# Kernel optimization log

Hardware: AMD Instinct MI355X
Metric: run time of the kernel (lower is better)

Reference implementation:

```python
import jax, jax.numpy as jnp
import numpy as np

E = 1024   # embd_size
H = 16     # head_count
HS = E // H
B = 8
T = 1024   # seq len == input_size
EPS = 1e-5

def _ln(x, g, b):
    m = jnp.mean(x, axis=-1, keepdims=True)
    v = jnp.mean((x - m) ** 2, axis=-1, keepdims=True)
    return (x - m) * jax.lax.rsqrt(v + EPS) * g + b

def setup_inputs() -> dict:
    key = jax.random.key(0)
    ks = jax.random.split(key, 12)
    s_attn = 1.0 / np.sqrt(E)
    s_ff1 = 1.0 / np.sqrt(E)
    s_ff2 = 1.0 / np.sqrt(4 * E)
    return {
        "x": jax.random.normal(ks[0], (B, T, E), dtype=jnp.float32),
        "wq": jax.random.normal(ks[1], (H, E, HS), dtype=jnp.float32) * s_attn,
        "wk": jax.random.normal(ks[2], (H, E, HS), dtype=jnp.float32) * s_attn,
        "wv": jax.random.normal(ks[3], (H, E, HS), dtype=jnp.float32) * s_attn,
        "w_proj": jax.random.normal(ks[4], (E, E), dtype=jnp.float32) * s_attn,
        "b_proj": jnp.zeros((E,), dtype=jnp.float32),
        "w1": jax.random.normal(ks[5], (E, 4 * E), dtype=jnp.float32) * s_ff1,
        "b1": jnp.zeros((4 * E,), dtype=jnp.float32),
        "w2": jax.random.normal(ks[6], (4 * E, E), dtype=jnp.float32) * s_ff2,
        "b2": jnp.zeros((E,), dtype=jnp.float32),
        "g1": jnp.ones((E,), dtype=jnp.float32),
        "be1": jnp.zeros((E,), dtype=jnp.float32),
        "g2": jnp.ones((E,), dtype=jnp.float32),
        "be2": jnp.zeros((E,), dtype=jnp.float32),
    }

def reference(x, wq, wk, wv, w_proj, b_proj, w1, b1, w2, b2, g1, be1, g2, be2):
    Tn = x.shape[1]
    h = _ln(x, g1, be1)
    # per-head projections, batched over heads: [B,T,E] x [H,E,S] -> [B,H,T,S]
    q = jnp.einsum('bte,hes->bhts', h, wq)
    k = jnp.einsum('bte,hes->bhts', h, wk)
    v = jnp.einsum('bte,hes->bhts', h, wv)
    scores = jnp.einsum('bhts,bhus->bhtu', q, k)
    # NOTE: source multiplies by sqrt(T) (x.shape[2] of scores), not 1/sqrt(head_size)
    scores = scores * jnp.float32(Tn) ** 0.5
    causal = jnp.tril(jnp.ones((Tn, Tn), dtype=bool))
    scores = jnp.where(causal, scores, -jnp.inf)
    attn = jax.nn.softmax(scores, axis=-1)
    out = jnp.einsum('bhtu,bhus->bhts', attn, v)           # [B,H,T,S]
    out = out.transpose(0, 2, 1, 3).reshape(x.shape[0], Tn, E)  # concat heads
    out = out @ w_proj + b_proj
    x = x + out
    f = _ln(x, g2, be2)
    f = jax.nn.relu(f @ w1 + b1) @ w2 + b2
    return x + f
```

## Files before the change

kernel.cpp:

```cpp
#include <hip/hip_runtime.h>


typedef unsigned short u16;
typedef __attribute__((ext_vector_type(8))) short  bfx8;
typedef __attribute__((ext_vector_type(4))) float  f32x4;
typedef __attribute__((ext_vector_type(4))) unsigned short u16v4;

#define MFMA16 __builtin_amdgcn_mfma_f32_16x16x32_bf16

__device__ __forceinline__ u16 f2bf(float f) {
    union { float f; unsigned u; } c; c.f = f;
    unsigned r = c.u + 0x7fffu + ((c.u >> 16) & 1u);
    return (u16)(r >> 16);
}
__device__ __forceinline__ float bf2f(u16 b) {
    union { unsigned u; float f; } c; c.u = ((unsigned)b) << 16; return c.f;
}
__device__ __forceinline__ float exp2_fast(float x) {
    float r; asm("v_exp_f32 %0, %1" : "=v"(r) : "v"(x)); return r;
}

__device__ __forceinline__ void gl_lds16(const void* g, void* l) {
    void* gg = (void*)g;
    __builtin_amdgcn_global_load_lds(
        (__attribute__((address_space(1))) void*)gg,
        (__attribute__((address_space(3))) void*)l,
        16, 0, 0);
}

__global__ __launch_bounds__(256)
void transpose_split(const float* __restrict__ src, u16* __restrict__ dhi,
                     u16* __restrict__ dlo, int C, int OS,
                     size_t inBS, size_t outBS)
{
    __shared__ float t[64][65];
    const int tid = threadIdx.x;
    const float* s = src + (size_t)blockIdx.z * inBS
                   + ((size_t)blockIdx.y * 64) * C + (size_t)blockIdx.x * 64;
    const size_t obase = (size_t)blockIdx.z * outBS
                       + ((size_t)blockIdx.x * 64) * OS + (size_t)blockIdx.y * 64;
    {
        const int r = tid >> 2, c4 = (tid & 3) * 16;
#pragma unroll
        for (int k = 0; k < 4; ++k) {
            float4 f = *(const float4*)(s + (size_t)r * C + c4 + k * 4);
            t[r][c4 + k*4 + 0] = f.x; t[r][c4 + k*4 + 1] = f.y;
            t[r][c4 + k*4 + 2] = f.z; t[r][c4 + k*4 + 3] = f.w;
        }
    }
    __syncthreads();
    {
        const int c = tid >> 2, r4 = (tid & 3) * 16;
        bfx8 h0, h1, l0, l1;
#pragma unroll
        for (int k = 0; k < 8; ++k) {
            float v0 = t[r4 + k][c];
            float v1 = t[r4 + 8 + k][c];
            u16 a = f2bf(v0), b = f2bf(v1);
            h0[k] = (short)a; h1[k] = (short)b;
            l0[k] = (short)f2bf(v0 - bf2f(a));
            l1[k] = (short)f2bf(v1 - bf2f(b));
        }
        u16* d = dhi + obase + (size_t)c * OS + r4;
        *(bfx8*)d = h0; *(bfx8*)(d + 8) = h1;
        if (dlo) {
            u16* d2 = dlo + obase + (size_t)c * OS + r4;
            *(bfx8*)d2 = l0; *(bfx8*)(d2 + 8) = l1;
        }
    }
}

__global__ __launch_bounds__(256)
void transpose_v(const u16* __restrict__ v, u16* __restrict__ vT)
{
    const int ut = blockIdx.x, h = blockIdx.y, b = blockIdx.z;
    __shared__ u16 t[64][72];
    const int tid = threadIdx.x;
    {
        const int u = tid >> 2, s4 = (tid & 3) * 16;
        const u16* src = v + ((size_t)(b * 1024 + ut * 64 + u)) * 1024 + h * 64 + s4;
        bfx8 a = *(const bfx8*)src;
        bfx8 c = *(const bfx8*)(src + 8);
#pragma unroll
        for (int k = 0; k < 8; ++k) { t[u][s4 + k] = (u16)a[k]; t[u][s4 + 8 + k] = (u16)c[k]; }
    }
    __syncthreads();
    {
        const int s = tid >> 2, u4 = (tid & 3) * 16;
        bfx8 o0, o1;
#pragma unroll
        for (int k = 0; k < 8; ++k) { o0[k] = (short)t[u4 + k][s]; o1[k] = (short)t[u4 + 8 + k][s]; }
        u16* dst = vT + ((size_t)((b * 16 + h) * 64 + s)) * 1024 + ut * 64 + u4;
        *(bfx8*)dst = o0; *(bfx8*)(dst + 8) = o1;
    }
}

__global__ __launch_bounds__(256)
void ln_split(const float* __restrict__ x, const float* __restrict__ g,
              const float* __restrict__ be, u16* __restrict__ hhi,
              u16* __restrict__ hlo)
{
    const int row = blockIdx.x;
    const int tid = threadIdx.x;
    const float4 v = ((const float4*)(x + (size_t)row * 1024))[tid];
    float s  = v.x + v.y + v.z + v.w;
    float s2 = v.x*v.x + v.y*v.y + v.z*v.z + v.w*v.w;
#pragma unroll
    for (int m = 32; m >= 1; m >>= 1) {
        s  += __shfl_xor(s,  m, 64);
        s2 += __shfl_xor(s2, m, 64);
    }
    __shared__ float rs[4], rq[4];
    if ((tid & 63) == 0) { rs[tid >> 6] = s; rq[tid >> 6] = s2; }
    __syncthreads();
    s  = rs[0] + rs[1] + rs[2] + rs[3];
    s2 = rq[0] + rq[1] + rq[2] + rq[3];
    const float mean = s * (1.0f / 1024.0f);
    const float var  = s2 * (1.0f / 1024.0f) - mean * mean;
    const float inv  = rsqrtf(var + 1e-5f);
    const int col0 = tid * 4;
    float hv[4];
    hv[0] = (v.x - mean) * inv * g[col0+0] + be[col0+0];
    hv[1] = (v.y - mean) * inv * g[col0+1] + be[col0+1];
    hv[2] = (v.z - mean) * inv * g[col0+2] + be[col0+2];
    hv[3] = (v.w - mean) * inv * g[col0+3] + be[col0+3];
    u16v4 hb, lb;
#pragma unroll
    for (int k = 0; k < 4; ++k) {
        u16 a = f2bf(hv[k]);
        hb[k] = a;
        lb[k] = f2bf(hv[k] - bf2f(a));
    }
    *(u16v4*)(hhi + (size_t)row * 1024 + col0) = hb;
    if (hlo) *(u16v4*)(hlo + (size_t)row * 1024 + col0) = lb;
}

#define BM 128
#define BN 128
#define BKT 32

template<int FLAGS>
__global__ __launch_bounds__(256, 2)
void gemm_bt(const u16* __restrict__ A, const u16* __restrict__ Bt,
             void* __restrict__ Cout, const float* __restrict__ bias,
             const float* __restrict__ res, int M, int N, int K)
{
    __shared__ u16 As[BM * BKT];
    __shared__ u16 Bs[BN * BKT];
    const int tid  = threadIdx.x;
    const int lane = tid & 63, wave = tid >> 6;
    const int wr = wave >> 1, wc = wave & 1;
    const int li = lane & 15, lg = lane >> 4;
    const size_t m0 = (size_t)blockIdx.y * BM;
    const size_t n0 = (size_t)blockIdx.x * BN;
    f32x4 acc[4][4] = {};

    const int slot0 = tid, slot1 = tid + 256;
    const int r0 = slot0 >> 2, kc0 = (slot0 & 3) * 8;
    const int r1 = slot1 >> 2, kc1 = (slot1 & 3) * 8;

    for (int kt = 0; kt < K; kt += BKT) {
        __syncthreads();
        gl_lds16(A  + (m0 + r0) * K + kt + kc0, As + slot0 * 8);
        gl_lds16(Bt + (n0 + r0) * K + kt + kc0, Bs + slot0 * 8);
        gl_lds16(A  + (m0 + r1) * K + kt + kc1, As + slot1 * 8);
        gl_lds16(Bt + (n0 + r1) * K + kt + kc1, Bs + slot1 * 8);
        __syncthreads();
        bfx8 af[4], bfr[4];
#pragma unroll
        for (int i = 0; i < 4; ++i)
            af[i] = *(const bfx8*)&As[(wr * 64 + i * 16 + li) * BKT + lg * 8];
#pragma unroll
        for (int j = 0; j < 4; ++j)
            bfr[j] = *(const bfx8*)&Bs[(wc * 64 + j * 16 + li) * BKT + lg * 8];
#pragma unroll
        for (int i = 0; i < 4; ++i)
#pragma unroll
            for (int j = 0; j < 4; ++j)
                acc[i][j] = MFMA16(af[i], bfr[j], acc[i][j], 0, 0, 0);
    }

    float* Cf = (float*)Cout;
    u16*   Cb = (u16*)Cout;
#pragma unroll
    for (int i = 0; i < 4; ++i)
#pragma unroll
        for (int j = 0; j < 4; ++j)
#pragma unroll
            for (int r = 0; r < 4; ++r) {
                const size_t row = m0 + wr * 64 + i * 16 + lg * 4 + r;
                const size_t col = n0 + wc * 64 + j * 16 + li;
                float v = acc[i][j][r];
                if (FLAGS & 1) v += bias[col];
                if (FLAGS & 2) v = fmaxf(v, 0.0f);
                if (FLAGS & 4) v += res[row * (size_t)N + col];
                if (FLAGS & 8) Cf[row * (size_t)N + col] = v;
                else           Cb[row * (size_t)N + col] = f2bf(v);
            }
}

__global__ __launch_bounds__(512, 2)
void gemm8_ffn1(const u16* __restrict__ A, const u16* __restrict__ Bt,
                u16* __restrict__ C, const float* __restrict__ bias,
                int M, int N, int K)
{
    __shared__ u16 Asl[2][2][128 * 64];
    __shared__ u16 Bsl[2][2][128 * 64];
    const int tid = threadIdx.x;
    const int lane = tid & 63, wave = tid >> 6;
    const int wr = wave >> 2, wc = wave & 3;
    const int li = lane & 15, lg = lane >> 4;

    const int bid = blockIdx.x;
    const int swz = (bid & 7) * 64 + (bid >> 3);
    const int bx = swz & 15, by = swz >> 4;
    const size_t m0 = (size_t)by * 256, n0 = (size_t)bx * 256;

    char* ldsA = (char*)&Asl[0][0][0];
    char* ldsB = (char*)&Bsl[0][0][0];

    auto stageA = [&](int j, int h) {
#pragma unroll
        for (int site = 0; site < 2; ++site) {
            const int s = tid + site * 512;
            const int r = s >> 3;
            const int cb = ((s & 7) << 4) ^ ((r & 7) << 4);
            gl_lds16((const char*)(A + (m0 + h * 128 + r) * (size_t)K + (size_t)j * 64) + cb,
                     ldsA + ((j & 1) * 2 + h) * 16384 + s * 16);
        }
    };
    auto stageB = [&](int j, int h) {
#pragma unroll
        for (int site = 0; site < 2; ++site) {
            const int s = tid + site * 512;
            const int r = s >> 3;
            const int cb = ((s & 7) << 4) ^ ((r & 7) << 4);
            gl_lds16((const char*)(Bt + (n0 + h * 128 + r) * (size_t)K + (size_t)j * 64) + cb,
                     ldsB + ((j & 1) * 2 + h) * 16384 + s * 16);
        }
    };

    const int lsw = (li & 7) << 4;
    const int aHalfBase = wr * 16384;
    const int bHalfBase = (wc >> 1) * 16384;
    const int bRow0 = (wc & 1) * 64;

    f32x4 acc[8][4] = {};
    const int NT = K >> 6;
    const int NI = NT >> 1;

    stageA(0, 0); stageA(0, 1); stageB(0, 0); stageB(0, 1);
    stageB(1, 0); stageB(1, 1);
    asm volatile("s_waitcnt vmcnt(0)" ::: "memory");
    __builtin_amdgcn_sched_barrier(0);
    __builtin_amdgcn_s_barrier();
    __builtin_amdgcn_sched_barrier(0);

    for (int t = 0; t < NI; ++t) {
        const bool more = (t + 1 < NI);
#pragma unroll
        for (int half = 0; half < 2; ++half) {
            const int buf = half;
            const int abase = buf * 32768 + aHalfBase;
            const int bbase = buf * 32768 + bHalfBase;
            bfx8 bfr[4][2];
#pragma unroll
            for (int q = 0; q < 4; ++q) {
                if (q == 0) {
#pragma unroll
                    for (int nf = 0; nf < 4; ++nf)
#pragma unroll
                        for (int ks = 0; ks < 2; ++ks)
                            bfr[nf][ks] = *(const bfx8*)(ldsB + bbase
                                + (bRow0 + nf * 16 + li) * 128
                                + ((ks * 64 + lg * 16) ^ lsw));
                }
                bfx8 afr[2][2];
#pragma unroll
                for (int m = 0; m < 2; ++m)
#pragma unroll
                    for (int ks = 0; ks < 2; ++ks)
                        afr[m][ks] = *(const bfx8*)(ldsA + abase
                            + ((2 * q + m) * 16 + li) * 128
                            + ((ks * 64 + lg * 16) ^ lsw));

                if (half == 0) {
                    if (q == 0) stageA(2 * t + 1, 0);
                    else if (q == 1) stageA(2 * t + 1, 1);
                    else if (q == 2) { if (more) stageB(2 * t + 2, 0); }
                    else             { if (more) stageB(2 * t + 2, 1); }
                } else {
                    if (q == 0)      { if (more) stageA(2 * t + 2, 0); }
                    else if (q == 1) { if (more) stageA(2 * t + 2, 1); }
                    else if (q == 2) { if (more) stageB(2 * t + 3, 0); }
                    else             { if (more) stageB(2 * t + 3, 1); }
                }

                __builtin_amdgcn_sched_barrier(0);
                __builtin_amdgcn_s_barrier();
                asm volatile("s_waitcnt lgkmcnt(0)" ::: "memory");
                __builtin_amdgcn_sched_barrier(0);
                __builtin_amdgcn_s_setprio(1);
#pragma unroll
                for (int ks = 0; ks < 2; ++ks)
#pragma unroll
                    for (int m = 0; m < 2; ++m)
#pragma unroll
                        for (int nf = 0; nf < 4; ++nf)
                            acc[2 * q + m][nf] = MFMA16(afr[m][ks], bfr[nf][ks],
                                                        acc[2 * q + m][nf], 0, 0, 0);
                __builtin_amdgcn_s_setprio(0);
                __builtin_amdgcn_sched_barrier(0);
                if (q == 3) {
                    if (half == 0) {
                        if (more) { asm volatile("s_waitcnt vmcnt(4)" ::: "memory"); }
                        else      { asm volatile("s_waitcnt vmcnt(0)" ::: "memory"); }
                    } else if (more) {
                        asm volatile("s_waitcnt vmcnt(4)" ::: "memory");
                    }
                    __builtin_amdgcn_sched_barrier(0);
                }
                __builtin_amdgcn_s_barrier();
                __builtin_amdgcn_sched_barrier(0);
            }
        }
    }

#pragma unroll
    for (int i = 0; i < 8; ++i)
#pragma unroll
        for (int nf = 0; nf < 4; ++nf)
#pragma unroll
            for (int r = 0; r < 4; ++r) {
                const size_t row = m0 + wr * 128 + i * 16 + lg * 4 + r;
                const size_t col = n0 + wc * 64 + nf * 16 + li;
                float v = acc[i][nf][r] + bias[col];
                v = fmaxf(v, 0.0f);
                C[row * (size_t)N + col] = f2bf(v);
            }
}

__global__ __launch_bounds__(256, 2)
void gemm_qk(const u16* __restrict__ Ah, const u16* __restrict__ Al,
             const u16* __restrict__ Bh, const u16* __restrict__ Bl,
             u16* __restrict__ Ohi, u16* __restrict__ Olo,
             int M, int N, int K)
{
    __shared__ u16 Ahs[BM * BKT], Als[BM * BKT], Bhs[BN * BKT], Bls[BN * BKT];
    const int tid  = threadIdx.x;
    const int lane = tid & 63, wave = tid >> 6;
    const int wr = wave >> 1, wc = wave & 1;
    const int li = lane & 15, lg = lane >> 4;
    const size_t m0 = (size_t)blockIdx.y * BM;
    const size_t n0 = (size_t)blockIdx.x * BN;
    f32x4 acc[4][4] = {};

    const int slot0 = tid, slot1 = tid + 256;
    const int r0 = slot0 >> 2, kc0 = (slot0 & 3) * 8;
    const int r1 = slot1 >> 2, kc1 = (slot1 & 3) * 8;

    for (int kt = 0; kt < K; kt += BKT) {
        __syncthreads();
        gl_lds16(Ah + (m0 + r0) * K + kt + kc0, Ahs + slot0 * 8);
        gl_lds16(Al + (m0 + r0) * K + kt + kc0, Als + slot0 * 8);
        gl_lds16(Bh + (n0 + r0) * K + kt + kc0, Bhs + slot0 * 8);
        gl_lds16(Bl + (n0 + r0) * K + kt + kc0, Bls + slot0 * 8);
        gl_lds16(Ah + (m0 + r1) * K + kt + kc1, Ahs + slot1 * 8);
        gl_lds16(Al + (m0 + r1) * K + kt + kc1, Als + slot1 * 8);
        gl_lds16(Bh + (n0 + r1) * K + kt + kc1, Bhs + slot1 * 8);
        gl_lds16(Bl + (n0 + r1) * K + kt + kc1, Bls + slot1 * 8);
        __syncthreads();
        bfx8 ah[4], al4[4], bh[4], bl4[4];
#pragma unroll
        for (int i = 0; i < 4; ++i) {
            ah[i]  = *(const bfx8*)&Ahs[(wr * 64 + i * 16 + li) * BKT + lg * 8];
            al4[i] = *(const bfx8*)&Als[(wr * 64 + i * 16 + li) * BKT + lg * 8];
        }
#pragma unroll
        for (int j = 0; j < 4; ++j) {
            bh[j]  = *(const bfx8*)&Bhs[(wc * 64 + j * 16 + li) * BKT + lg * 8];
            bl4[j] = *(const bfx8*)&Bls[(wc * 64 + j * 16 + li) * BKT + lg * 8];
        }
#pragma unroll
        for (int i = 0; i < 4; ++i)
#pragma unroll
            for (int j = 0; j < 4; ++j) {
                acc[i][j] = MFMA16(ah[i],  bh[j],  acc[i][j], 0, 0, 0);
                acc[i][j] = MFMA16(ah[i],  bl4[j], acc[i][j], 0, 0, 0);
                acc[i][j] = MFMA16(al4[i], bh[j],  acc[i][j], 0, 0, 0);
            }
    }
#pragma unroll
    for (int i = 0; i < 4; ++i)
#pragma unroll
        for (int j = 0; j < 4; ++j)
#pragma unroll
            for (int r = 0; r < 4; ++r) {
                const size_t row = m0 + wr * 64 + i * 16 + lg * 4 + r;
                const size_t col = n0 + wc * 64 + j * 16 + li;
                const float v = acc[i][j][r];
                const u16 hi = f2bf(v);
                Ohi[row * (size_t)N + col] = hi;
                Olo[row * (size_t)N + col] = f2bf(v - bf2f(hi));
            }
}

#define QKS 2048

__global__ __launch_bounds__(256, 3)
void attn(const u16* __restrict__ qkhi, const u16* __restrict__ qklo,
          const u16* __restrict__ vt, u16* __restrict__ ao)
{
    const int id  = blockIdx.x;
    const int swz = (id & 7) * 256 + (id >> 3);
    const int qt  = 15 - (swz & 15);
    const int h   = (swz >> 4) & 15;
    const int b   = swz >> 8;

    const int tid = threadIdx.x;
    const int wave = tid >> 6, lane = tid & 63;
    const int li = lane & 15, lg = lane >> 4;

    __shared__ u16 KsHi[2][4096];
    __shared__ u16 KsLo[2][4096];
    __shared__ u16 Pl[64 * 64];

    const size_t qrow = (size_t)b * 1024 + qt * 64 + wave * 16 + li;
    const size_t qoff = qrow * QKS + h * 64 + lg * 8;
    const bfx8 qh0 = *(const bfx8*)(qkhi + qoff);
    const bfx8 qh1 = *(const bfx8*)(qkhi + qoff + 32);
    const bfx8 ql0 = *(const bfx8*)(qklo + qoff);
    const bfx8 ql1 = *(const bfx8*)(qklo + qoff + 32);

    bfx8 onesf;
#pragma unroll
    for (int k = 0; k < 8; ++k) onesf[k] = (short)0x3F80;

    f32x4 O[4] = {};
    f32x4 O5 = {0.f, 0.f, 0.f, 0.f};
    float mrow[4] = {-3e38f, -3e38f, -3e38f, -3e38f};

    const u16* kh_base = qkhi + ((size_t)b * 1024) * QKS + 1024 + h * 64;
    const u16* kl_base = qklo + ((size_t)b * 1024) * QKS + 1024 + h * 64;
    const u16* v_base  = vt + ((size_t)(b * 16 + h) * 64) * 1024;

    auto stageK = [&](int kt, int bufIdx) {
#pragma unroll
        for (int site = 0; site < 2; ++site) {
            const int s = tid + site * 256;
            const int r = s >> 3;
            const int cb = (((s & 7) << 4) ^ ((r & 7) << 4));
            const size_t go = ((size_t)(kt * 64 + r)) * QKS;
            gl_lds16((const char*)(kh_base + go) + cb, (char*)&KsHi[bufIdx][0] + s * 16);
            gl_lds16((const char*)(kl_base + go) + cb, (char*)&KsLo[bufIdx][0] + s * 16);
        }
    };

    const int rswz = (li & 7) << 4;
    char* pband = (char*)&Pl[0] + wave * 2048;

    stageK(0, 0);

    for (int kt = 0; kt <= qt; ++kt) {
        const int cur = kt & 1;

        bfx8 vld[2][4];
#pragma unroll
        for (int nf = 0; nf < 4; ++nf) {
            const u16* vr = v_base + ((size_t)(nf * 16 + li)) * 1024 + kt * 64 + lg * 8;
            vld[0][nf] = *(const bfx8*)vr;
            vld[1][nf] = *(const bfx8*)(vr + 32);
        }

        if (kt < qt) {
            stageK(kt + 1, cur ^ 1);
            asm volatile("s_waitcnt vmcnt(12)" ::: "memory");
        } else {
            asm volatile("s_waitcnt vmcnt(8)" ::: "memory");
        }
        __builtin_amdgcn_sched_barrier(0);
        __builtin_amdgcn_s_barrier();
        __builtin_amdgcn_sched_barrier(0);

        float sv[4][4];
        const char* khc = (const char*)&KsHi[cur][0];
        const char* klc = (const char*)&KsLo[cur][0];
#pragma unroll
        for (int nf = 0; nf < 4; ++nf) {
            const int rb = (nf * 16 + li) * 128;
            bfx8 kh0v = *(const bfx8*)(khc + rb + (((lg * 16) + 0 ) ^ rswz));
            bfx8 kh1v = *(const bfx8*)(khc + rb + (((lg * 16) + 64) ^ rswz));
            bfx8 kl0v = *(const bfx8*)(klc + rb + (((lg * 16) + 0 ) ^ rswz));
            bfx8 kl1v = *(const bfx8*)(klc + rb + (((lg * 16) + 64) ^ rswz));
            f32x4 a = {0.f, 0.f, 0.f, 0.f};
            a = MFMA16(qh0, kh0v, a, 0, 0, 0);
            a = MFMA16(qh1, kh1v, a, 0, 0, 0);
            a = MFMA16(qh0, kl0v, a, 0, 0, 0);
            a = MFMA16(qh1, kl1v, a, 0, 0, 0);
            a = MFMA16(ql0, kh0v, a, 0, 0, 0);
            a = MFMA16(ql1, kh1v, a, 0, 0, 0);
#pragma unroll
            for (int r = 0; r < 4; ++r) sv[nf][r] = a[r];
        }

        asm volatile("s_waitcnt lgkmcnt(0)" ::: "memory");
        __builtin_amdgcn_sched_barrier(0);
        __builtin_amdgcn_s_barrier();
        __builtin_amdgcn_sched_barrier(0);

        const float SC = 46.16624130844683f;
        float pmax[4] = {-3e38f, -3e38f, -3e38f, -3e38f};
        if (kt == qt) {
            const int rowg = qt * 64 + wave * 16 + lg * 4;
            const int colg = kt * 64 + li;
#pragma unroll
            for (int nf = 0; nf < 4; ++nf)
#pragma unroll
                for (int r = 0; r < 4; ++r) {
                    float x2 = sv[nf][r] * SC;
                    if (colg + nf * 16 > rowg + r) x2 = -3e38f;
                    sv[nf][r] = x2;
                    pmax[r] = fmaxf(pmax[r], x2);
                }
        } else {
#pragma unroll
            for (int nf = 0; nf < 4; ++nf)
#pragma unroll
                for (int r = 0; r < 4; ++r) {
                    const float x2 = sv[nf][r] * SC;
                    sv[nf][r] = x2;
                    pmax[r] = fmaxf(pmax[r], x2);
                }
        }
#pragma unroll
        for (int msk = 1; msk < 16; msk <<= 1)
#pragma unroll
            for (int r = 0; r < 4; ++r)
                pmax[r] = fmaxf(pmax[r], __shfl_xor(pmax[r], msk, 64));

        const bool grow = !__all((pmax[0] - mrow[0] <= 11.5416f) &&
                                 (pmax[1] - mrow[1] <= 11.5416f) &&
                                 (pmax[2] - mrow[2] <= 11.5416f) &&
                                 (pmax[3] - mrow[3] <= 11.5416f));
        if (grow) {
            float alr[4];
#pragma unroll
            for (int r = 0; r < 4; ++r) {
                const float mnew = fmaxf(mrow[r], pmax[r]);
                alr[r] = exp2_fast(mrow[r] - mnew);
                mrow[r] = mnew;
            }
#pragma unroll
            for (int nf = 0; nf < 4; ++nf)
#pragma unroll
                for (int r = 0; r < 4; ++r)
                    O[nf][r] *= alr[r];
#pragma unroll
            for (int r = 0; r < 4; ++r)
                O5[r] *= alr[r];
        }

#pragma unroll
        for (int nf = 0; nf < 4; ++nf)
#pragma unroll
            for (int r = 0; r < 4; ++r) {
                const int prow = lg * 4 + r;
                const int pb = prow * 128 + ((((nf * 16 + li) * 2)) ^ ((prow & 7) << 4));
                *(u16*)(pband + pb) = f2bf(exp2_fast(sv[nf][r] - mrow[r]));
            }

#pragma unroll
        for (int ku = 0; ku < 2; ++ku) {
            bfx8 pf = *(const bfx8*)(pband + li * 128
                                     + ((ku * 64 + lg * 16) ^ ((li & 7) << 4)));
#pragma unroll
            for (int nf = 0; nf < 4; ++nf)
                O[nf] = MFMA16(pf, vld[ku][nf], O[nf], 0, 0, 0);
            O5 = MFMA16(pf, onesf, O5, 0, 0, 0);
        }
    }

    float invl[4];
#pragma unroll
    for (int r = 0; r < 4; ++r) invl[r] = 1.0f / O5[r];
    const size_t orow = (size_t)b * 1024 + qt * 64 + wave * 16 + lg * 4;
#pragma unroll
    for (int nf = 0; nf < 4; ++nf)
#pragma unroll
        for (int r = 0; r < 4; ++r)
            ao[(orow + r) * 1024 + h * 64 + nf * 16 + li] = f2bf(O[nf][r] * invl[r]);
}

extern "C" void kernel_launch(void* const* d_in, const int* in_sizes, int n_in,
                              void* d_out, int out_size, void* d_ws, size_t ws_size,
                              hipStream_t stream)
{
    (void)in_sizes; (void)n_in; (void)out_size; (void)ws_size;
    const float* x      = (const float*)d_in[0];
    const float* wq     = (const float*)d_in[1];
    const float* wk     = (const float*)d_in[2];
    const float* wv     = (const float*)d_in[3];
    const float* w_proj = (const float*)d_in[4];
    const float* b_proj = (const float*)d_in[5];
    const float* w1     = (const float*)d_in[6];
    const float* b1     = (const float*)d_in[7];
    const float* w2     = (const float*)d_in[8];
    const float* b2     = (const float*)d_in[9];
    const float* g1     = (const float*)d_in[10];
    const float* be1    = (const float*)d_in[11];
    const float* g2     = (const float*)d_in[12];
    const float* be2    = (const float*)d_in[13];
    float* out = (float*)d_out;

    const size_t MB = (size_t)1024 * 1024;
    char* wsp = (char*)d_ws;
    u16* h_hi  = (u16*)(wsp + 0 * MB);
    u16* h_lo  = (u16*)(wsp + 16 * MB);
    u16* qk_hi = (u16*)(wsp + 32 * MB);
    u16* qk_lo = (u16*)(wsp + 64 * MB);
    u16* v_b   = (u16*)(wsp + 96 * MB);
    u16* vtr   = (u16*)(wsp + 112 * MB);
    float* y   = (float*)(wsp + 128 * MB);
    u16* wqkT_hi = (u16*)(wsp + 160 * MB);
    u16* wqkT_lo = (u16*)(wsp + 164 * MB);
    u16* wvT     = (u16*)(wsp + 168 * MB);
    u16* wpT     = (u16*)(wsp + 170 * MB);
    u16* w1T     = (u16*)(wsp + 172 * MB);
    u16* w2T     = (u16*)(wsp + 180 * MB);
    u16* f2  = h_hi;
    u16* ao  = h_lo;
    u16* act = qk_hi;

    dim3 blk(256);

    transpose_split<<<dim3(1, 16, 16), blk, 0, stream>>>(wq, wqkT_hi, wqkT_lo, 64, 1024, (size_t)65536, (size_t)65536);
    transpose_split<<<dim3(1, 16, 16), blk, 0, stream>>>(wk, wqkT_hi + (size_t)1024 * 1024, wqkT_lo + (size_t)1024 * 1024, 64, 1024, (size_t)65536, (size_t)65536);
    transpose_split<<<dim3(1, 16, 16), blk, 0, stream>>>(wv, wvT, nullptr, 64, 1024, (size_t)65536, (size_t)65536);
    transpose_split<<<dim3(16, 16, 1), blk, 0, stream>>>(w_proj, wpT, nullptr, 1024, 1024, 0, 0);
    transpose_split<<<dim3(64, 16, 1), blk, 0, stream>>>(w1, w1T, nullptr, 4096, 1024, 0, 0);
    transpose_split<<<dim3(16, 64, 1), blk, 0, stream>>>(w2, w2T, nullptr, 1024, 4096, 0, 0);

    ln_split<<<8192, blk, 0, stream>>>(x, g1, be1, h_hi, h_lo);

    gemm_qk<<<dim3(16, 64), blk, 0, stream>>>(h_hi, h_lo, wqkT_hi, wqkT_lo, qk_hi, qk_lo, 8192, 2048, 1024);
    gemm_bt<0><<<dim3(8, 64), blk, 0, stream>>>(h_hi, wvT, v_b, nullptr, nullptr, 8192, 1024, 1024);
    transpose_v<<<dim3(16, 16, 8), blk, 0, stream>>>(v_b, vtr);

    attn<<<dim3(2048), blk, 0, stream>>>(qk_hi, qk_lo, vtr, ao);

    gemm_bt<1 | 4 | 8><<<dim3(8, 64), blk, 0, stream>>>(ao, wpT, y, b_proj, x, 8192, 1024, 1024);

    ln_split<<<8192, blk, 0, stream>>>(y, g2, be2, f2, nullptr);

    gemm8_ffn1<<<dim3(512), dim3(512), 0, stream>>>(f2, w1T, act, b1, 8192, 4096, 1024);
    gemm_bt<1 | 4 | 8><<<dim3(8, 64), blk, 0, stream>>>(act, w2T, out, b2, y, 8192, 1024, 4096);
}
```

Measured before the change: 547.1 us.

## Run split-bf16 QK projection through the pipelined 256x256 gemm8 kernel

Generalizes the FFN1 256x256 double-buffered LDS-pipelined GEMM into a template with an optional split3 mode. In that mode the K loop is extended to three passes (hi*hi, hi*lo, lo*hi) over concatenated tiles. This replaces the simple 128x128 gemm_qk kernel for the Q/K projection, aiming for better data reuse and load/compute overlap. The cost is a grid of only 256 blocks, which may underfill the GPU, and more complex tile-source selection per stage.

```diff
diff --git a/kernel.cpp b/kernel.cpp
--- a/kernel.cpp
+++ b/kernel.cpp
@@ -199,10 +199,13 @@
             }
 }
 
+template<int EPI, int SPLIT3>
 __global__ __launch_bounds__(512, 2)
-void gemm8_ffn1(const u16* __restrict__ A, const u16* __restrict__ Bt,
-                u16* __restrict__ C, const float* __restrict__ bias,
-                int M, int N, int K)
+void gemm8(const u16* __restrict__ A, const u16* __restrict__ Al,
+           const u16* __restrict__ Bt, const u16* __restrict__ Bl,
+           u16* __restrict__ C, u16* __restrict__ Clo,
+           const float* __restrict__ bias,
+           int M, int N, int K, int NBX)
 {
     __shared__ u16 Asl[2][2][128 * 64];
     __shared__ u16 Bsl[2][2][128 * 64];
@@ -212,30 +215,46 @@
     const int li = lane & 15, lg = lane >> 4;
 
     const int bid = blockIdx.x;
-    const int swz = (bid & 7) * 64 + (bid >> 3);
-    const int bx = swz & 15, by = swz >> 4;
+    const int nwg = gridDim.x;
+    const int cpx = nwg >> 3;
+    const int swz = (bid & 7) * cpx + (bid >> 3);
+    const int bx = swz % NBX, by = swz / NBX;
     const size_t m0 = (size_t)by * 256, n0 = (size_t)bx * 256;
 
     char* ldsA = (char*)&Asl[0][0][0];
     char* ldsB = (char*)&Bsl[0][0][0];
 
+    const int KT = K >> 6;
+
     auto stageA = [&](int j, int h) {
+        const u16* src = A;
+        int jj = j;
+        if (SPLIT3) {
+            src = (j < 2 * KT) ? A : Al;
+            jj = (j < KT) ? j : ((j < 2 * KT) ? j - KT : j - 2 * KT);
+        }
 #pragma unroll
         for (int site = 0; site < 2; ++site) {
             const int s = tid + site * 512;
             const int r = s >> 3;
             const int cb = ((s & 7) << 4) ^ ((r & 7) << 4);
-            gl_lds16((const char*)(A + (m0 + h * 128 + r) * (size_t)K + (size_t)j * 64) + cb,
+            gl_lds16((const char*)(src + (m0 + h * 128 + r) * (size_t)K + (size_t)jj * 64) + cb,
                      ldsA + ((j & 1) * 2 + h) * 16384 + s * 16);
         }
     };
     auto stageB = [&](int j, int h) {
+        const u16* src = Bt;
+        int jj = j;
+        if (SPLIT3) {
+            src = (j < KT) ? Bt : ((j < 2 * KT) ? Bl : Bt);
+            jj = (j < KT) ? j : ((j < 2 * KT) ? j - KT : j - 2 * KT);
+        }
 #pragma unroll
         for (int site = 0; site < 2; ++site) {
             const int s = tid + site * 512;
             const int r = s >> 3;
             const int cb = ((s & 7) << 4) ^ ((r & 7) << 4);
-            gl_lds16((const char*)(Bt + (n0 + h * 128 + r) * (size_t)K + (size_t)j * 64) + cb,
+            gl_lds16((const char*)(src + (n0 + h * 128 + r) * (size_t)K + (size_t)jj * 64) + cb,
                      ldsB + ((j & 1) * 2 + h) * 16384 + s * 16);
         }
     };
@@ -246,7 +265,7 @@
     const int bRow0 = (wc & 1) * 64;
 
     f32x4 acc[8][4] = {};
-    const int NT = K >> 6;
+    const int NT = SPLIT3 ? 3 * KT : KT;
     const int NI = NT >> 1;
 
     stageA(0, 0); stageA(0, 1); stageB(0, 0); stageB(0, 1);
@@ -334,74 +353,16 @@
             for (int r = 0; r < 4; ++r) {
                 const size_t row = m0 + wr * 128 + i * 16 + lg * 4 + r;
                 const size_t col = n0 + wc * 64 + nf * 16 + li;
-                float v = acc[i][nf][r] + bias[col];
-                v = fmaxf(v, 0.0f);
-                C[row * (size_t)N + col] = f2bf(v);
-            }
-}
-
-__global__ __launch_bounds__(256, 2)
-void gemm_qk(const u16* __restrict__ Ah, const u16* __restrict__ Al,
-             const u16* __restrict__ Bh, const u16* __restrict__ Bl,
-             u16* __restrict__ Ohi, u16* __restrict__ Olo,
-             int M, int N, int K)
-{
-    __shared__ u16 Ahs[BM * BKT], Als[BM * BKT], Bhs[BN * BKT], Bls[BN * BKT];
-    const int tid  = threadIdx.x;
-    const int lane = tid & 63, wave = tid >> 6;
-    const int wr = wave >> 1, wc = wave & 1;
-    const int li = lane & 15, lg = lane >> 4;
-    const size_t m0 = (size_t)blockIdx.y * BM;
-    const size_t n0 = (size_t)blockIdx.x * BN;
-    f32x4 acc[4][4] = {};
-
-    const int slot0 = tid, slot1 = tid + 256;
-    const int r0 = slot0 >> 2, kc0 = (slot0 & 3) * 8;
-    const int r1 = slot1 >> 2, kc1 = (slot1 & 3) * 8;
-
-    for (int kt = 0; kt < K; kt += BKT) {
-        __syncthreads();
-        gl_lds16(Ah + (m0 + r0) * K + kt + kc0, Ahs + slot0 * 8);
-        gl_lds16(Al + (m0 + r0) * K + kt + kc0, Als + slot0 * 8);
-        gl_lds16(Bh + (n0 + r0) * K + kt + kc0, Bhs + slot0 * 8);
-        gl_lds16(Bl + (n0 + r0) * K + kt + kc0, Bls + slot0 * 8);
-        gl_lds16(Ah + (m0 + r1) * K + kt + kc1, Ahs + slot1 * 8);
-        gl_lds16(Al + (m0 + r1) * K + kt + kc1, Als + slot1 * 8);
-        gl_lds16(Bh + (n0 + r1) * K + kt + kc1, Bhs + slot1 * 8);
-        gl_lds16(Bl + (n0 + r1) * K + kt + kc1, Bls + slot1 * 8);
-        __syncthreads();
-        bfx8 ah[4], al4[4], bh[4], bl4[4];
-#pragma unroll
-        for (int i = 0; i < 4; ++i) {
-            ah[i]  = *(const bfx8*)&Ahs[(wr * 64 + i * 16 + li) * BKT + lg * 8];
-            al4[i] = *(const bfx8*)&Als[(wr * 64 + i * 16 + li) * BKT + lg * 8];
-        }
-#pragma unroll
-        for (int j = 0; j < 4; ++j) {
-            bh[j]  = *(const bfx8*)&Bhs[(wc * 64 + j * 16 + li) * BKT + lg * 8];
-            bl4[j] = *(const bfx8*)&Bls[(wc * 64 + j * 16 + li) * BKT + lg * 8];
-        }
-#pragma unroll
-        for (int i = 0; i < 4; ++i)
-#pragma unroll
-            for (int j = 0; j < 4; ++j) {
-                acc[i][j] = MFMA16(ah[i],  bh[j],  acc[i][j], 0, 0, 0);
-                acc[i][j] = MFMA16(ah[i],  bl4[j], acc[i][j], 0, 0, 0);
-                acc[i][j] = MFMA16(al4[i], bh[j],  acc[i][j], 0, 0, 0);
-            }
-    }
-#pragma unroll
-    for (int i = 0; i < 4; ++i)
-#pragma unroll
-        for (int j = 0; j < 4; ++j)
-#pragma unroll
-            for (int r = 0; r < 4; ++r) {
-                const size_t row = m0 + wr * 64 + i * 16 + lg * 4 + r;
-                const size_t col = n0 + wc * 64 + j * 16 + li;
-                const float v = acc[i][j][r];
-                const u16 hi = f2bf(v);
-                Ohi[row * (size_t)N + col] = hi;
-                Olo[row * (size_t)N + col] = f2bf(v - bf2f(hi));
+                if (EPI == 0) {
+                    float v = acc[i][nf][r] + bias[col];
+                    v = fmaxf(v, 0.0f);
+                    C[row * (size_t)N + col] = f2bf(v);
+                } else {
+                    const float v = acc[i][nf][r];
+                    const u16 hi = f2bf(v);
+                    C[row * (size_t)N + col]   = hi;
+                    Clo[row * (size_t)N + col] = f2bf(v - bf2f(hi));
+                }
             }
 }
 
@@ -642,7 +603,9 @@
 
     ln_split<<<8192, blk, 0, stream>>>(x, g1, be1, h_hi, h_lo);
 
-    gemm_qk<<<dim3(16, 64), blk, 0, stream>>>(h_hi, h_lo, wqkT_hi, wqkT_lo, qk_hi, qk_lo, 8192, 2048, 1024);
+    gemm8<1, 1><<<dim3(256), dim3(512), 0, stream>>>(h_hi, h_lo, wqkT_hi, wqkT_lo,
+                                                     qk_hi, qk_lo, nullptr,
+                                                     8192, 2048, 1024, 8);
     gemm_bt<0><<<dim3(8, 64), blk, 0, stream>>>(h_hi, wvT, v_b, nullptr, nullptr, 8192, 1024, 1024);
     transpose_v<<<dim3(16, 16, 8), blk, 0, stream>>>(v_b, vtr);
 
@@ -652,6 +615,8 @@
 
     ln_split<<<8192, blk, 0, stream>>>(y, g2, be2, f2, nullptr);
 
-    gemm8_ffn1<<<dim3(512), dim3(512), 0, stream>>>(f2, w1T, act, b1, 8192, 4096, 1024);
+    gemm8<0, 0><<<dim3(512), dim3(512), 0, stream>>>(f2, nullptr, w1T, nullptr,
+                                                     act, nullptr, b1,
+                                                     8192, 4096, 1024, 16);
     gemm_bt<1 | 4 | 8><<<dim3(8, 64), blk, 0, stream>>>(act, w2T, out, b2, y, 8192, 1024, 4096);
 }
```

Result: faster. 522.6 us (-4.5%).
